# Optimization experiments

Hardware: AMD Instinct MI355X
Metric: run time of the kernel (lower is better)

## Reference

```python
import jax, jax.numpy as jnp
import numpy as np

MASK_VALUE = -1000000000.0
N = 100000        # num nodes
E = 1600000       # num edges
IN_DIM = 128
HID = 128
MAXN = 100000     # max_num_nodes
TAU = 0.5


def setup_inputs() -> dict:
    key = jax.random.key(0)
    ks = jax.random.split(key, 24)
    s_in = 1.0 / np.sqrt(IN_DIM)
    s_h = 1.0 / np.sqrt(HID)
    s_2h = 1.0 / np.sqrt(2 * HID)
    return {
        "x": jax.random.normal(ks[0], (N, IN_DIM), jnp.float32),
        "edge_index": jax.random.randint(ks[1], (2, E), 0, N, jnp.int32),
        # GCN layer params (PyG GCNConv: lin weight + bias)
        "W1": jax.random.normal(ks[2], (IN_DIM, HID), jnp.float32) * s_in,
        "b1": jnp.zeros((HID,), jnp.float32),
        "W2": jax.random.normal(ks[3], (HID, HID), jnp.float32) * s_h,
        "b2": jnp.zeros((HID,), jnp.float32),
        "W3": jax.random.normal(ks[4], (HID, HID), jnp.float32) * s_h,
        "b3": jnp.zeros((HID,), jnp.float32),
        # heads
        "n1W": jax.random.normal(ks[5], (2 * HID, MAXN), jnp.float32) * s_2h,
        "n1b": jnp.zeros((MAXN,), jnp.float32),
        "n2W": jax.random.normal(ks[6], (2 * HID, MAXN), jnp.float32) * s_2h,
        "n2b": jnp.zeros((MAXN,), jnp.float32),
        "eW": jax.random.normal(ks[7], (2 * HID, 3), jnp.float32) * s_2h,
        "eb": jnp.zeros((3,), jnp.float32),
        "sW": jax.random.normal(ks[8], (2 * HID, 1), jnp.float32) * s_2h,
        "sb": jnp.zeros((1,), jnp.float32),
        # gumbel noise for the 4 gumbel_softmax calls (deterministic reference)
        "g1": jax.random.gumbel(ks[9], (1, MAXN), jnp.float32),
        "g2": jax.random.gumbel(ks[10], (1, MAXN), jnp.float32),
        "ge": jax.random.gumbel(ks[11], (1, 3), jnp.float32),
        "gs": jax.random.gumbel(ks[12], (1, 1), jnp.float32),
    }


def _gcn_layer(x, W, b, src, dst, n):
    # PyG GCNConv: self-loops + symmetric norm D^-1/2 (A+I) D^-1/2 (XW) + b
    h = x @ W                                            # [n, H]
    deg = jnp.zeros((n,), h.dtype).at[dst].add(1.0) + 1.0  # +1 self-loop
    dinv = jax.lax.rsqrt(deg)
    msg = h[src] * (dinv[src] * dinv[dst])[:, None]      # [E, H] gather
    out = jax.ops.segment_sum(msg, dst, num_segments=n)  # scatter-add at targets
    out = out + h * (dinv * dinv)[:, None]               # self-loop contribution
    return out + b


def _gumbel_softmax(logits, g):
    return jax.nn.softmax((logits + g) / TAU, axis=-1)


def _mask_logits(logits, n, prev_idx, src, dst):
    # logits: [1, MAXN]
    idx = jnp.arange(logits.shape[-1])
    logits = jnp.where(idx[None, :] >= n, MASK_VALUE, logits)
    if prev_idx is not None:
        m = (src == prev_idx) | (dst == prev_idx)
        conn = jnp.zeros((logits.shape[-1],), bool)
        # scatter True at connected nodes; unmatched edges map onto prev_idx
        conn = conn.at[jnp.where(m, src, prev_idx)].set(True)
        conn = conn.at[jnp.where(m, dst, prev_idx)].set(True)
        conn = conn.at[prev_idx].set(True)
        logits = jnp.where(conn[None, :], MASK_VALUE, logits)
    return logits


def reference(x, edge_index, W1, b1, W2, b2, W3, b3, n1W, n1b, n2W, n2b, eW, eb, sW, sb, g1, g2, ge, gs):
    src, dst = edge_index[0], edge_index[1]
    n = x.shape[0]
    h = jax.nn.relu(_gcn_layer(x, W1, b1, src, dst, n))
    h = jax.nn.relu(_gcn_layer(h, W2, b2, src, dst, n))
    gcn = jax.nn.relu(_gcn_layer(h, W3, b3, src, dst, n))   # [n, H]

    pool = jnp.concatenate([gcn.mean(0, keepdims=True), gcn.max(0, keepdims=True)], axis=1)  # [1, 2H]

    l1 = _mask_logits(pool @ n1W + n1b, n, None, src, dst)
    n1_soft = _gumbel_softmax(l1, g1)                      # [1, MAXN]
    i1 = jnp.argmax(n1_soft, axis=-1)[0]

    l2 = _mask_logits(pool @ n2W + n2b, n, i1, src, dst)
    n2_soft = _gumbel_softmax(l2, g2)
    i2 = jnp.argmax(n2_soft, axis=-1)[0]

    node_emb = jnp.concatenate([gcn[i1][None, :], gcn[i2][None, :]], axis=1)  # [1, 2H]
    e_soft = _gumbel_softmax(node_emb @ eW + eb, ge)       # [1, 3]
    s_soft = _gumbel_softmax(pool @ sW + sb, gs)           # [1, 1]
    return (n1_soft, n2_soft, e_soft, s_soft)
```

## Files before the change

### kernel.cpp

```cpp
#include <hip/hip_runtime.h>

#define HID 128
#define MASKV -1000000000.0f
#define INV_TAU 2.0f
#define NB_SHIFT 9
#define NBMAX 256
#define ECHUNK 4096
#define BCAP 10240
#define FP8_SCALE 16.0f
#define FP8_INV_SCALE 0.0625f

using short8 = __attribute__((ext_vector_type(8))) short;
using f32x4  = __attribute__((ext_vector_type(4))) float;
using f32x2  = __attribute__((ext_vector_type(2))) float;

__device__ inline ushort f2bf(float f) {
  unsigned u = __float_as_uint(f);
  return (ushort)((u + 0x7FFFu + ((u >> 16) & 1u)) >> 16);
}
__device__ inline float bflo(unsigned u) { return __uint_as_float(u << 16); }
__device__ inline float bfhi(unsigned u) { return __uint_as_float(u & 0xFFFF0000u); }

__device__ inline unsigned char f2fp8(float v) {
  int p = __builtin_amdgcn_cvt_pk_fp8_f32(v, v, 0, false);
  return (unsigned char)(p & 0xFF);
}
__device__ inline void acc_fp8x4(unsigned w, float& a0, float& a1, float& a2, float& a3) {
  f32x2 lo = __builtin_amdgcn_cvt_pk_f32_fp8((int)w, false);
  f32x2 hi = __builtin_amdgcn_cvt_pk_f32_fp8((int)w, true);
  a0 += lo[0]; a1 += lo[1]; a2 += hi[0]; a3 += hi[1];
}

__device__ inline unsigned ordered_bits(float f) {
  unsigned u = __float_as_uint(f);
  return (u & 0x80000000u) ? ~u : (u | 0x80000000u);
}
__device__ inline int key_idx(unsigned long long k) {
  return (int)(0xFFFFFFFFu - (unsigned)(k & 0xFFFFFFFFull));
}

__global__ __launch_bounds__(256) void prep(uint4* __restrict__ zp, int n16, int* __restrict__ bcur, int zb,
                                            const float* __restrict__ W1, const float* __restrict__ W2,
                                            const float* __restrict__ W3, ushort* __restrict__ Wt) {
  int b = blockIdx.x, t = threadIdx.x;
  if (b == 0) { bcur[t] = t * BCAP; return; }
  if (b <= zb) {
    int i = (b - 1) * 256 + t;
    if (i < n16) zp[i] = make_uint4(0u, 0u, 0u, 0u);
    return;
  }
  int cb = b - zb - 1;
  const float* W = (cb < 64) ? W1 : (cb < 128) ? W2 : W3;
  ushort* o = Wt + (size_t)(cb >> 6) * 128 * 128;
  int idx = (cb & 63) * 256 + t;
  int c = idx >> 7, k = idx & 127;
  o[idx] = f2bf(W[k * 128 + c]);
}

__global__ __launch_bounds__(256) void edge_bucket(const int* __restrict__ ei, int E, int nb,
                                                   int* __restrict__ bcur, unsigned* __restrict__ staged) {
  __shared__ unsigned spk[ECHUNK];
  __shared__ unsigned char sbk[ECHUNK];
  __shared__ int hist[NBMAX];
  __shared__ int cur[NBMAX];
  int t = threadIdx.x;
  int e0 = blockIdx.x * ECHUNK;
  int cnt = min(ECHUNK, E - e0);
  if (t < nb) hist[t] = 0;
  __syncthreads();
  for (int i = t; i < cnt; i += 256) {
    int s = ei[e0 + i];
    int d = ei[E + e0 + i];
    int b = d >> NB_SHIFT;
    spk[i] = ((unsigned)(d & ((1 << NB_SHIFT) - 1)) << 23) | (unsigned)s;
    sbk[i] = (unsigned char)b;
    atomicAdd(&hist[b], 1);
  }
  __syncthreads();
  if (t < nb) cur[t] = atomicAdd(&bcur[t], hist[t]);
  __syncthreads();
  for (int i = t; i < cnt; i += 256) {
    int b = sbk[i];
    int pos = atomicAdd(&cur[b], 1);
    staged[pos] = spk[i];
  }
}

__global__ __launch_bounds__(512) void bucket_csr2(const unsigned* __restrict__ staged, const int* __restrict__ bcur,
                                                   int* __restrict__ rows, int* __restrict__ cnt,
                                                   float* __restrict__ dinv, int* __restrict__ col, int n) {
  __shared__ int lcnt[512];
  __shared__ int lgs[512];
  __shared__ int lcur[512];
  __shared__ int lsc[512];
  int b = blockIdx.x;
  int t = threadIdx.x;
  int base = b << NB_SHIFT;
  lcnt[t] = 0;
  lcur[t] = 0;
  __syncthreads();
  int start = b * BCAP;
  int end = bcur[b];
  for (int i = start + t; i < end; i += 512) {
    atomicAdd(&lcnt[staged[i] >> 23], 1);
  }
  __syncthreads();
  int v = lcnt[t];
  lsc[t] = v;
  __syncthreads();
  for (int d = 1; d < 512; d <<= 1) {
    int x = (t >= d) ? lsc[t - d] : 0;
    __syncthreads();
    lsc[t] += x;
    __syncthreads();
  }
  int gstart = start + lsc[t] - v;
  lgs[t] = gstart;
  int node = base + t;
  if (node < n) {
    rows[node] = gstart;
    cnt[node] = v;
    dinv[node] = rsqrtf((float)v + 1.0f);
  }
  __syncthreads();
  for (int i = start + t; i < end; i += 512) {
    unsigned p = staged[i];
    int dl = (int)(p >> 23);
    int pos = atomicAdd(&lcur[dl], 1);
    col[lgs[dl] + pos] = (int)(p & 0x7FFFFFu);
  }
}

__global__ __launch_bounds__(256) void mfma_gemm(const float* __restrict__ Ain, const ushort* __restrict__ Wt,
                                                 const float* __restrict__ dinv, unsigned char* __restrict__ hW8, int n) {
  int w = threadIdx.x >> 6;
  int l = threadIdx.x & 63;
  int lr = l & 15;
  int lg = l >> 4;
  int r0 = blockIdx.x * 64 + w * 16;
  if (r0 >= n) return;
  int arow = r0 + lr;
  if (arow >= n) arow = n - 1;

  f32x4 acc[8];
#pragma unroll
  for (int ct = 0; ct < 8; ++ct) acc[ct] = (f32x4){0.f, 0.f, 0.f, 0.f};

#pragma unroll
  for (int kk = 0; kk < 4; ++kk) {
    const float* Af = Ain + (size_t)arow * 128 + kk * 32 + lg * 8;
    float4 f0 = ((const float4*)Af)[0];
    float4 f1 = ((const float4*)Af)[1];
    short8 a;
    a[0] = (short)f2bf(f0.x); a[1] = (short)f2bf(f0.y);
    a[2] = (short)f2bf(f0.z); a[3] = (short)f2bf(f0.w);
    a[4] = (short)f2bf(f1.x); a[5] = (short)f2bf(f1.y);
    a[6] = (short)f2bf(f1.z); a[7] = (short)f2bf(f1.w);
#pragma unroll
    for (int ct = 0; ct < 8; ++ct) {
      short8 bfrag = ((const short8*)(Wt + (size_t)(ct * 16 + lr) * 128))[kk * 4 + lg];
      acc[ct] = __builtin_amdgcn_mfma_f32_16x16x32_bf16(a, bfrag, acc[ct], 0, 0, 0);
    }
  }

#pragma unroll
  for (int r = 0; r < 4; ++r) {
    int row = r0 + lg * 4 + r;
    if (row < n) {
      float dv = dinv[row] * FP8_SCALE;
#pragma unroll
      for (int ct = 0; ct < 8; ++ct) {
        hW8[(size_t)row * 128 + ct * 16 + lr] = f2fp8(acc[ct][r] * dv);
      }
    }
  }
}

template <int DO_GEMM>
__global__ __launch_bounds__(512) void gather_fuse(const int* __restrict__ row_start, const int* __restrict__ cnt,
                                                   const int* __restrict__ col, const unsigned char* __restrict__ hW8in,
                                                   const float* __restrict__ dinv, const float* __restrict__ bias,
                                                   const ushort* __restrict__ Wt_next, unsigned char* __restrict__ hW8out,
                                                   ushort* __restrict__ gcn_out, int n) {
  __shared__ ushort lh[16][136];
  int t = threadIdx.x;
  int grp = t >> 5, lane = t & 31;
  int g = blockIdx.x * 16 + grp;
  bool valid = g < n;
  int gc = valid ? g : (n - 1);
  const unsigned* h32 = (const unsigned*)hW8in;
  float a0 = 0.f, a1 = 0.f, a2 = 0.f, a3 = 0.f;
  acc_fp8x4(h32[(size_t)gc * 32 + lane], a0, a1, a2, a3);
  int jb = row_start[gc];
  int je = jb + cnt[gc];
  int j = jb;
  for (; j + 4 <= je; j += 4) {
    int s0 = __builtin_nontemporal_load(col + j);
    int s1 = __builtin_nontemporal_load(col + j + 1);
    int s2 = __builtin_nontemporal_load(col + j + 2);
    int s3 = __builtin_nontemporal_load(col + j + 3);
    unsigned w0 = h32[(size_t)s0 * 32 + lane];
    unsigned w1 = h32[(size_t)s1 * 32 + lane];
    unsigned w2 = h32[(size_t)s2 * 32 + lane];
    unsigned w3 = h32[(size_t)s3 * 32 + lane];
    acc_fp8x4(w0, a0, a1, a2, a3);
    acc_fp8x4(w1, a0, a1, a2, a3);
    acc_fp8x4(w2, a0, a1, a2, a3);
    acc_fp8x4(w3, a0, a1, a2, a3);
  }
  for (; j < je; ++j) {
    int s0 = __builtin_nontemporal_load(col + j);
    unsigned w0 = h32[(size_t)s0 * 32 + lane];
    acc_fp8x4(w0, a0, a1, a2, a3);
  }
  float din = dinv[gc] * FP8_INV_SCALE;
  float4 bb = ((const float4*)bias)[lane];
  a0 = fmaxf(fmaf(a0, din, bb.x), 0.f);
  a1 = fmaxf(fmaf(a1, din, bb.y), 0.f);
  a2 = fmaxf(fmaf(a2, din, bb.z), 0.f);
  a3 = fmaxf(fmaf(a3, din, bb.w), 0.f);
  if (!valid) { a0 = a1 = a2 = a3 = 0.f; }

  if (DO_GEMM) {
    ushort* dl = &lh[grp][lane * 4];
    dl[0] = f2bf(a0); dl[1] = f2bf(a1); dl[2] = f2bf(a2); dl[3] = f2bf(a3);
    __syncthreads();
    int w = t >> 6;
    int l = t & 63;
    int lr = l & 15, lg = l >> 4;
    f32x4 acc = (f32x4){0.f, 0.f, 0.f, 0.f};
#pragma unroll
    for (int kk = 0; kk < 4; ++kk) {
      short8 a = *(const short8*)(&lh[lr][kk * 32 + lg * 8]);
      short8 bfrag = ((const short8*)(Wt_next + (size_t)(w * 16 + lr) * 128))[kk * 4 + lg];
      acc = __builtin_amdgcn_mfma_f32_16x16x32_bf16(a, bfrag, acc, 0, 0, 0);
    }
    int r0 = blockIdx.x * 16;
#pragma unroll
    for (int r = 0; r < 4; ++r) {
      int row = r0 + lg * 4 + r;
      if (row < n) {
        float dv = dinv[row] * FP8_SCALE;
        hW8out[(size_t)row * 128 + w * 16 + lr] = f2fp8(acc[r] * dv);
      }
    }
  } else {
    if (valid) {
      ushort4 o = {f2bf(a0), f2bf(a1), f2bf(a2), f2bf(a3)};
      *(ushort4*)(gcn_out + (size_t)g * 128 + lane * 4) = o;
    }
  }
}

#define POOL_GRID 512
__global__ __launch_bounds__(256) void pool_kernel(const ushort* __restrict__ gcn, float* __restrict__ psum,
                                                   float* __restrict__ pmax, int nrows) {
  __shared__ float ls[16 * 128];
  __shared__ float lm[16 * 128];
  int t = threadIdx.x;
  int g = t >> 4;
  int c = t & 15;
  float s0 = 0.f, s1 = 0.f, s2 = 0.f, s3 = 0.f, s4 = 0.f, s5 = 0.f, s6 = 0.f, s7 = 0.f;
  float m0 = 0.f, m1 = 0.f, m2 = 0.f, m3 = 0.f, m4 = 0.f, m5 = 0.f, m6 = 0.f, m7 = 0.f;
  for (int r = blockIdx.x * 16 + g; r < nrows; r += POOL_GRID * 16) {
    uint4 w = *(const uint4*)(gcn + (size_t)r * 128 + c * 8);
    float v0 = bflo(w.x), v1 = bfhi(w.x), v2 = bflo(w.y), v3 = bfhi(w.y);
    float v4 = bflo(w.z), v5 = bfhi(w.z), v6 = bflo(w.w), v7 = bfhi(w.w);
    s0 += v0; s1 += v1; s2 += v2; s3 += v3; s4 += v4; s5 += v5; s6 += v6; s7 += v7;
    m0 = fmaxf(m0, v0); m1 = fmaxf(m1, v1); m2 = fmaxf(m2, v2); m3 = fmaxf(m3, v3);
    m4 = fmaxf(m4, v4); m5 = fmaxf(m5, v5); m6 = fmaxf(m6, v6); m7 = fmaxf(m7, v7);
  }
  int cb = c * 8;
  ls[g * 128 + cb + 0] = s0; ls[g * 128 + cb + 1] = s1; ls[g * 128 + cb + 2] = s2; ls[g * 128 + cb + 3] = s3;
  ls[g * 128 + cb + 4] = s4; ls[g * 128 + cb + 5] = s5; ls[g * 128 + cb + 6] = s6; ls[g * 128 + cb + 7] = s7;
  lm[g * 128 + cb + 0] = m0; lm[g * 128 + cb + 1] = m1; lm[g * 128 + cb + 2] = m2; lm[g * 128 + cb + 3] = m3;
  lm[g * 128 + cb + 4] = m4; lm[g * 128 + cb + 5] = m5; lm[g * 128 + cb + 6] = m6; lm[g * 128 + cb + 7] = m7;
  __syncthreads();
  if (t < 128) {
    float s = 0.f, m = 0.f;
#pragma unroll
    for (int gg = 0; gg < 16; ++gg) {
      s += ls[gg * 128 + t];
      m = fmaxf(m, lm[gg * 128 + t]);
    }
    atomicAdd(&psum[t], s);
    atomicMax((unsigned*)&pmax[t], __float_as_uint(m));
  }
}

__global__ __launch_bounds__(256) void head_fused(const float* __restrict__ W, const float* __restrict__ bias,
                                                  const float* __restrict__ g, const float* __restrict__ psum,
                                                  const float* __restrict__ pmax, float invn,
                                                  const int* __restrict__ conn, int use_conn,
                                                  float* __restrict__ ebuf, unsigned long long* __restrict__ cell,
                                                  float* __restrict__ sum, int maxn, int n) {
  __shared__ float p[256];
  __shared__ unsigned long long kred[256];
  __shared__ float sred[256];
  int t = threadIdx.x;
  p[t] = (t < 128) ? psum[t] * invn : pmax[t - 128];
  __syncthreads();
  int j0 = blockIdx.x * 512 + t;
  int j1 = j0 + 256;
  bool v0 = j0 < maxn, v1 = j1 < maxn;
  float acc0 = 0.f, acc1 = 0.f;
#pragma unroll 8
  for (int k = 0; k < 256; ++k) {
    const float* row = W + (size_t)k * maxn;
    float w0 = v0 ? __builtin_nontemporal_load(row + j0) : 0.f;
    float w1 = v1 ? __builtin_nontemporal_load(row + j1) : 0.f;
    acc0 = fmaf(p[k], w0, acc0);
    acc1 = fmaf(p[k], w1, acc1);
  }
  unsigned long long key = 0ull;
  float evs = 0.f;
  if (v0) {
    float logit = acc0 + bias[j0];
    if (j0 >= n) logit = MASKV;
    if (use_conn && conn[j0]) logit = MASKV;
    float zv = (logit + g[j0]) * INV_TAU;
    float ev = expf(zv);
    ebuf[j0] = ev;
    evs += ev;
    unsigned long long k0 = ((unsigned long long)ordered_bits(zv) << 32) | (unsigned long long)(0xFFFFFFFFu - (unsigned)j0);
    key = k0;
  }
  if (v1) {
    float logit = acc1 + bias[j1];
    if (j1 >= n) logit = MASKV;
    if (use_conn && conn[j1]) logit = MASKV;
    float zv = (logit + g[j1]) * INV_TAU;
    float ev = expf(zv);
    ebuf[j1] = ev;
    evs += ev;
    unsigned long long k1 = ((unsigned long long)ordered_bits(zv) << 32) | (unsigned long long)(0xFFFFFFFFu - (unsigned)j1);
    key = key > k1 ? key : k1;
  }
  kred[t] = key;
  sred[t] = evs;
  __syncthreads();
  for (int s = 128; s > 0; s >>= 1) {
    if (t < s) {
      kred[t] = kred[t] > kred[t + s] ? kred[t] : kred[t + s];
      sred[t] += sred[t + s];
    }
    __syncthreads();
  }
  if (t == 0) {
    atomicMax(cell, kred[0]);
    atomicAdd(sum, sred[0]);
  }
}

__global__ __launch_bounds__(256) void conn_kernel(const int* __restrict__ ei, int E,
                                                   const unsigned long long* __restrict__ cell1,
                                                   int* __restrict__ conn) {
  int e = blockIdx.x * 256 + threadIdx.x;
  int i1 = key_idx(*cell1);
  if (e == 0) conn[i1] = 1;
  if (e < E) {
    int s = ei[e], d = ei[E + e];
    if (s == i1 || d == i1) {
      conn[s] = 1;
      conn[d] = 1;
    }
  }
}

__device__ void edge_stop(const ushort* __restrict__ gcn, const float* __restrict__ eW,
                          const float* __restrict__ ebias, const float* __restrict__ ge,
                          const unsigned long long* __restrict__ c1, const unsigned long long* __restrict__ c2,
                          float* __restrict__ ob) {
  __shared__ float red[3 * 128];
  int t = threadIdx.x;
  if (t < 128) {
    int i1 = key_idx(*c1);
    int i2 = key_idx(*c2);
    float ea  = __uint_as_float((unsigned)gcn[(size_t)i1 * HID + t] << 16);
    float eb2 = __uint_as_float((unsigned)gcn[(size_t)i2 * HID + t] << 16);
    red[t]       = ea * eW[t * 3 + 0] + eb2 * eW[(128 + t) * 3 + 0];
    red[128 + t] = ea * eW[t * 3 + 1] + eb2 * eW[(128 + t) * 3 + 1];
    red[256 + t] = ea * eW[t * 3 + 2] + eb2 * eW[(128 + t) * 3 + 2];
  }
  __syncthreads();
  for (int s = 64; s > 0; s >>= 1) {
    if (t < s) {
      red[t] += red[t + s];
      red[128 + t] += red[128 + t + s];
      red[256 + t] += red[256 + t + s];
    }
    __syncthreads();
  }
  if (t == 0) {
    float z0 = (red[0]   + ebias[0] + ge[0]) * INV_TAU;
    float z1 = (red[128] + ebias[1] + ge[1]) * INV_TAU;
    float z2 = (red[256] + ebias[2] + ge[2]) * INV_TAU;
    float m = fmaxf(z0, fmaxf(z1, z2));
    float e0 = expf(z0 - m), e1 = expf(z1 - m), e2 = expf(z2 - m);
    float inv = 1.f / (e0 + e1 + e2);
    ob[0] = e0 * inv;
    ob[1] = e1 * inv;
    ob[2] = e2 * inv;
    ob[3] = 1.0f;
  }
}

__global__ __launch_bounds__(256) void finish(const float* __restrict__ e1, const float* __restrict__ s1,
                                              const float* __restrict__ e2, const float* __restrict__ s2,
                                              float* __restrict__ out, int maxn,
                                              const ushort* __restrict__ gcn, const float* __restrict__ eW,
                                              const float* __restrict__ ebias, const float* __restrict__ ge,
                                              const unsigned long long* __restrict__ c1,
                                              const unsigned long long* __restrict__ c2) {
  if (blockIdx.x == gridDim.x - 1) {
    edge_stop(gcn, eW, ebias, ge, c1, c2, out + 2 * (size_t)maxn);
    return;
  }
  int j = blockIdx.x * 256 + threadIdx.x;
  if (j < maxn) {
    out[j] = e1[j] / (*s1);
    out[maxn + j] = e2[j] / (*s2);
  }
}

extern "C" void kernel_launch(void* const* d_in, const int* in_sizes, int n_in,
                              void* d_out, int out_size, void* d_ws, size_t ws_size,
                              hipStream_t stream) {
  const float* x  = (const float*)d_in[0];
  const int* ei   = (const int*)d_in[1];
  const float* W1 = (const float*)d_in[2];
  const float* b1 = (const float*)d_in[3];
  const float* W2 = (const float*)d_in[4];
  const float* b2 = (const float*)d_in[5];
  const float* W3 = (const float*)d_in[6];
  const float* b3 = (const float*)d_in[7];
  const float* n1W = (const float*)d_in[8];
  const float* n1b = (const float*)d_in[9];
  const float* n2W = (const float*)d_in[10];
  const float* n2b = (const float*)d_in[11];
  const float* eW  = (const float*)d_in[12];
  const float* eb  = (const float*)d_in[13];
  const float* g1  = (const float*)d_in[16];
  const float* g2  = (const float*)d_in[17];
  const float* ge  = (const float*)d_in[18];

  int n    = in_sizes[0] / HID;
  int E    = in_sizes[1] / 2;
  int maxn = in_sizes[9];
  int nb   = (n + (1 << NB_SHIFT) - 1) >> NB_SHIFT;
  float* out = (float*)d_out;

  char* ws = (char*)d_ws;
  size_t o = 0;
  unsigned char* HW8A = (unsigned char*)(ws + o); o += (size_t)n * HID;
  unsigned char* HW8B = (unsigned char*)(ws + o); o += (size_t)n * HID;
  ushort* GCN = (ushort*)(ws + o); o += (size_t)n * HID * 2;
  ushort* WT  = (ushort*)(ws + o); o += (size_t)3 * 128 * 128 * 2;
  float* EB1  = (float*)(ws + o);  o += (size_t)maxn * 4;
  float* EB2  = (float*)(ws + o);  o += (size_t)maxn * 4;
  int* ROWS   = (int*)(ws + o);    o += (size_t)n * 4;
  int* CNT    = (int*)(ws + o);    o += (size_t)n * 4;
  int* COL    = (int*)(ws + o);    o += (size_t)NBMAX * BCAP * 4;
  unsigned* STAGED = (unsigned*)(ws + o); o += (size_t)NBMAX * BCAP * 4;
  float* DINV = (float*)(ws + o);  o += (size_t)n * 4;
  int* BCUR   = (int*)(ws + o);    o += 1024;
  char* zero_start = ws + o;
  int* CONN   = (int*)(ws + o);    o += (size_t)maxn * 4;
  float* PS   = (float*)(ws + o);  o += 128 * 4;
  float* PM   = (float*)(ws + o);  o += 128 * 4;
  unsigned long long* CELLS = (unsigned long long*)(ws + o);
  float* SUM1 = (float*)(ws + o + 16);
  float* SUM2 = (float*)(ws + o + 20);
  o += 64;
  size_t zero_bytes = (size_t)((ws + o) - zero_start);
  int zero16 = (int)(zero_bytes / 16);
  int zb = (zero16 + 255) / 256;

  dim3 blk(256);
  int gE = (E + 255) / 256;
  int gHeadHalf = (maxn + 511) / 512;
  int gNorm = (maxn + 255) / 256;
  int gGemm = (n + 63) / 64;
  int gFuse = (n + 15) / 16;
  int gEB = (E + ECHUNK - 1) / ECHUNK;
  float invn = 1.0f / (float)n;

  prep<<<1 + zb + 192, blk, 0, stream>>>((uint4*)zero_start, zero16, BCUR, zb, W1, W2, W3, WT);

  edge_bucket<<<gEB, blk, 0, stream>>>(ei, E, nb, BCUR, STAGED);
  bucket_csr2<<<nb, dim3(512), 0, stream>>>(STAGED, BCUR, ROWS, CNT, DINV, COL, n);

  mfma_gemm<<<gGemm, blk, 0, stream>>>(x, WT, DINV, HW8A, n);
  gather_fuse<1><<<gFuse, dim3(512), 0, stream>>>(ROWS, CNT, COL, HW8A, DINV, b1, WT + 128 * 128, HW8B, nullptr, n);
  gather_fuse<1><<<gFuse, dim3(512), 0, stream>>>(ROWS, CNT, COL, HW8B, DINV, b2, WT + 2 * 128 * 128, HW8A, nullptr, n);
  gather_fuse<0><<<gFuse, dim3(512), 0, stream>>>(ROWS, CNT, COL, HW8A, DINV, b3, nullptr, nullptr, GCN, n);

  pool_kernel<<<POOL_GRID, blk, 0, stream>>>(GCN, PS, PM, n);

  head_fused<<<gHeadHalf, blk, 0, stream>>>(n1W, n1b, g1, PS, PM, invn, nullptr, 0, EB1, &CELLS[0], SUM1, maxn, n);

  conn_kernel<<<gE, blk, 0, stream>>>(ei, E, &CELLS[0], CONN);

  head_fused<<<gHeadHalf, blk, 0, stream>>>(n2W, n2b, g2, PS, PM, invn, CONN, 1, EB2, &CELLS[1], SUM2, maxn, n);

  finish<<<gNorm + 1, blk, 0, stream>>>(EB1, SUM1, EB2, SUM2, out, maxn, GCN, eW, eb, ge, &CELLS[0], &CELLS[1]);
}
```

Baseline: 392.5 us.

## Split fused gather+GEMM into separate gather and FP8-input GEMM kernels

Unfuses the per-layer gather-aggregate and next-layer GEMM. Each gather kernel now writes post-ReLU activations as scaled FP8 to an intermediate buffer, and a separate gemm8 kernel converts them back to bf16 for MFMA with the next weight matrix. This removes the block-wide __syncthreads and the shared-memory staging from the gather kernel, letting gather run at 256 threads with early exit. The cost is two extra kernel launches and an extra round trip of n*128 bytes per layer.

```diff
diff --git a/kernel.cpp b/kernel.cpp
--- a/kernel.cpp
+++ b/kernel.cpp
@@ -24,6 +24,11 @@
 __device__ inline unsigned char f2fp8(float v) {
   int p = __builtin_amdgcn_cvt_pk_fp8_f32(v, v, 0, false);
   return (unsigned char)(p & 0xFF);
+}
+__device__ inline unsigned pk4_fp8(float a0, float a1, float a2, float a3) {
+  int w0 = __builtin_amdgcn_cvt_pk_fp8_f32(a0, a1, 0, false);
+  int w1 = __builtin_amdgcn_cvt_pk_fp8_f32(a2, a3, 0, false);
+  return (unsigned)(w0 & 0xFFFF) | ((unsigned)(w1 & 0xFFFF) << 16);
 }
 __device__ inline void acc_fp8x4(unsigned w, float& a0, float& a1, float& a2, float& a3) {
   f32x2 lo = __builtin_amdgcn_cvt_pk_f32_fp8((int)w, false);
@@ -176,23 +181,67 @@
   }
 }
 
-template <int DO_GEMM>
-__global__ __launch_bounds__(512) void gather_fuse(const int* __restrict__ row_start, const int* __restrict__ cnt,
-                                                   const int* __restrict__ col, const unsigned char* __restrict__ hW8in,
-                                                   const float* __restrict__ dinv, const float* __restrict__ bias,
-                                                   const ushort* __restrict__ Wt_next, unsigned char* __restrict__ hW8out,
-                                                   ushort* __restrict__ gcn_out, int n) {
-  __shared__ ushort lh[16][136];
-  int t = threadIdx.x;
-  int grp = t >> 5, lane = t & 31;
-  int g = blockIdx.x * 16 + grp;
-  bool valid = g < n;
-  int gc = valid ? g : (n - 1);
-  const unsigned* h32 = (const unsigned*)hW8in;
+__global__ __launch_bounds__(256) void gemm8(const unsigned char* __restrict__ Hf8, const ushort* __restrict__ Wt,
+                                             const float* __restrict__ dinv, unsigned char* __restrict__ hW8, int n) {
+  int w = threadIdx.x >> 6;
+  int l = threadIdx.x & 63;
+  int lr = l & 15;
+  int lg = l >> 4;
+  int r0 = blockIdx.x * 64 + w * 16;
+  if (r0 >= n) return;
+  int arow = r0 + lr;
+  if (arow >= n) arow = n - 1;
+  const uint2* Arow = (const uint2*)(Hf8 + (size_t)arow * 128);
+
+  f32x4 acc[8];
+#pragma unroll
+  for (int ct = 0; ct < 8; ++ct) acc[ct] = (f32x4){0.f, 0.f, 0.f, 0.f};
+
+#pragma unroll
+  for (int kk = 0; kk < 4; ++kk) {
+    uint2 a8 = Arow[kk * 4 + lg];
+    f32x2 p0 = __builtin_amdgcn_cvt_pk_f32_fp8((int)a8.x, false);
+    f32x2 p1 = __builtin_amdgcn_cvt_pk_f32_fp8((int)a8.x, true);
+    f32x2 p2 = __builtin_amdgcn_cvt_pk_f32_fp8((int)a8.y, false);
+    f32x2 p3 = __builtin_amdgcn_cvt_pk_f32_fp8((int)a8.y, true);
+    short8 a;
+    a[0] = (short)f2bf(p0[0]); a[1] = (short)f2bf(p0[1]);
+    a[2] = (short)f2bf(p1[0]); a[3] = (short)f2bf(p1[1]);
+    a[4] = (short)f2bf(p2[0]); a[5] = (short)f2bf(p2[1]);
+    a[6] = (short)f2bf(p3[0]); a[7] = (short)f2bf(p3[1]);
+#pragma unroll
+    for (int ct = 0; ct < 8; ++ct) {
+      short8 bfrag = ((const short8*)(Wt + (size_t)(ct * 16 + lr) * 128))[kk * 4 + lg];
+      acc[ct] = __builtin_amdgcn_mfma_f32_16x16x32_bf16(a, bfrag, acc[ct], 0, 0, 0);
+    }
+  }
+
+#pragma unroll
+  for (int r = 0; r < 4; ++r) {
+    int row = r0 + lg * 4 + r;
+    if (row < n) {
+      float dv = dinv[row];
+#pragma unroll
+      for (int ct = 0; ct < 8; ++ct) {
+        hW8[(size_t)row * 128 + ct * 16 + lr] = f2fp8(acc[ct][r] * dv);
+      }
+    }
+  }
+}
+
+template <int OUTFP8>
+__global__ __launch_bounds__(256) void gather_k(const int* __restrict__ row_start, const int* __restrict__ cnt,
+                                                const int* __restrict__ col, const unsigned char* __restrict__ hW8,
+                                                const float* __restrict__ dinv, const float* __restrict__ bias,
+                                                void* __restrict__ outp, int n) {
+  int g = (blockIdx.x * 256 + threadIdx.x) >> 5;
+  if (g >= n) return;
+  int lane = threadIdx.x & 31;
+  const unsigned* h32 = (const unsigned*)hW8;
   float a0 = 0.f, a1 = 0.f, a2 = 0.f, a3 = 0.f;
-  acc_fp8x4(h32[(size_t)gc * 32 + lane], a0, a1, a2, a3);
-  int jb = row_start[gc];
-  int je = jb + cnt[gc];
+  acc_fp8x4(h32[(size_t)g * 32 + lane], a0, a1, a2, a3);
+  int jb = row_start[g];
+  int je = jb + cnt[g];
   int j = jb;
   for (; j + 4 <= je; j += 4) {
     int s0 = __builtin_nontemporal_load(col + j);
@@ -213,42 +262,18 @@
     unsigned w0 = h32[(size_t)s0 * 32 + lane];
     acc_fp8x4(w0, a0, a1, a2, a3);
   }
-  float din = dinv[gc] * FP8_INV_SCALE;
+  float din = dinv[g] * FP8_INV_SCALE;
   float4 bb = ((const float4*)bias)[lane];
   a0 = fmaxf(fmaf(a0, din, bb.x), 0.f);
   a1 = fmaxf(fmaf(a1, din, bb.y), 0.f);
   a2 = fmaxf(fmaf(a2, din, bb.z), 0.f);
   a3 = fmaxf(fmaf(a3, din, bb.w), 0.f);
-  if (!valid) { a0 = a1 = a2 = a3 = 0.f; }
-
-  if (DO_GEMM) {
-    ushort* dl = &lh[grp][lane * 4];
-    dl[0] = f2bf(a0); dl[1] = f2bf(a1); dl[2] = f2bf(a2); dl[3] = f2bf(a3);
-    __syncthreads();
-    int w = t >> 6;
-    int l = t & 63;
-    int lr = l & 15, lg = l >> 4;
-    f32x4 acc = (f32x4){0.f, 0.f, 0.f, 0.f};
-#pragma unroll
-    for (int kk = 0; kk < 4; ++kk) {
-      short8 a = *(const short8*)(&lh[lr][kk * 32 + lg * 8]);
-      short8 bfrag = ((const short8*)(Wt_next + (size_t)(w * 16 + lr) * 128))[kk * 4 + lg];
-      acc = __builtin_amdgcn_mfma_f32_16x16x32_bf16(a, bfrag, acc, 0, 0, 0);
-    }
-    int r0 = blockIdx.x * 16;
-#pragma unroll
-    for (int r = 0; r < 4; ++r) {
-      int row = r0 + lg * 4 + r;
-      if (row < n) {
-        float dv = dinv[row] * FP8_SCALE;
-        hW8out[(size_t)row * 128 + w * 16 + lr] = f2fp8(acc[r] * dv);
-      }
-    }
+  if (OUTFP8) {
+    unsigned wo = pk4_fp8(a0 * FP8_SCALE, a1 * FP8_SCALE, a2 * FP8_SCALE, a3 * FP8_SCALE);
+    ((unsigned*)outp)[(size_t)g * 32 + lane] = wo;
   } else {
-    if (valid) {
-      ushort4 o = {f2bf(a0), f2bf(a1), f2bf(a2), f2bf(a3)};
-      *(ushort4*)(gcn_out + (size_t)g * 128 + lane * 4) = o;
-    }
+    ushort4 o = {f2bf(a0), f2bf(a1), f2bf(a2), f2bf(a3)};
+    *(ushort4*)((ushort*)outp + (size_t)g * 128 + lane * 4) = o;
   }
 }
 
@@ -454,6 +479,7 @@
   size_t o = 0;
   unsigned char* HW8A = (unsigned char*)(ws + o); o += (size_t)n * HID;
   unsigned char* HW8B = (unsigned char*)(ws + o); o += (size_t)n * HID;
+  unsigned char* HF8  = (unsigned char*)(ws + o); o += (size_t)n * HID;
   ushort* GCN = (ushort*)(ws + o); o += (size_t)n * HID * 2;
   ushort* WT  = (ushort*)(ws + o); o += (size_t)3 * 128 * 128 * 2;
   float* EB1  = (float*)(ws + o);  o += (size_t)maxn * 4;
@@ -481,7 +507,7 @@
   int gHeadHalf = (maxn + 511) / 512;
   int gNorm = (maxn + 255) / 256;
   int gGemm = (n + 63) / 64;
-  int gFuse = (n + 15) / 16;
+  int gGather = (int)(((size_t)n * 32 + 255) / 256);
   int gEB = (E + ECHUNK - 1) / ECHUNK;
   float invn = 1.0f / (float)n;
 
@@ -491,9 +517,11 @@
   bucket_csr2<<<nb, dim3(512), 0, stream>>>(STAGED, BCUR, ROWS, CNT, DINV, COL, n);
 
   mfma_gemm<<<gGemm, blk, 0, stream>>>(x, WT, DINV, HW8A, n);
-  gather_fuse<1><<<gFuse, dim3(512), 0, stream>>>(ROWS, CNT, COL, HW8A, DINV, b1, WT + 128 * 128, HW8B, nullptr, n);
-  gather_fuse<1><<<gFuse, dim3(512), 0, stream>>>(ROWS, CNT, COL, HW8B, DINV, b2, WT + 2 * 128 * 128, HW8A, nullptr, n);
-  gather_fuse<0><<<gFuse, dim3(512), 0, stream>>>(ROWS, CNT, COL, HW8A, DINV, b3, nullptr, nullptr, GCN, n);
+  gather_k<1><<<gGather, blk, 0, stream>>>(ROWS, CNT, COL, HW8A, DINV, b1, HF8, n);
+  gemm8<<<gGemm, blk, 0, stream>>>(HF8, WT + 128 * 128, DINV, HW8B, n);
+  gather_k<1><<<gGather, blk, 0, stream>>>(ROWS, CNT, COL, HW8B, DINV, b2, HF8, n);
+  gemm8<<<gGemm, blk, 0, stream>>>(HF8, WT + 2 * 128 * 128, DINV, HW8A, n);
+  gather_k<0><<<gGather, blk, 0, stream>>>(ROWS, CNT, COL, HW8A, DINV, b3, GCN, n);
 
   pool_kernel<<<POOL_GRID, blk, 0, stream>>>(GCN, PS, PM, n);
 
```

Measured after the change: 399.9 us. Within noise of the previous version (+1.9%).
